# Optimization experiments

Measured on AMD Instinct MI355X. Metric: run time of the kernel, lower is better.

## Reference

```python
import jax, jax.numpy as jnp
import numpy as np

SEQ_LEN, INPUT_DIM, HIDDEN_DIM, NUM_CLASSES, BATCH = 512, 256, 1024, 128, 256


def setup_inputs() -> dict:
    key = jax.random.key(0)
    ks = jax.random.split(key, 12)
    sx = np.sqrt(2.0 / INPUT_DIM).astype(np.float32)
    sh = np.sqrt(2.0 / HIDDEN_DIM).astype(np.float32)
    inp = {
        "x": jax.random.randint(ks[0], (BATCH, SEQ_LEN, 1), 0, NUM_CLASSES, dtype=jnp.int32),
        "emb": jax.random.normal(ks[1], (NUM_CLASSES, INPUT_DIM), jnp.float32),
        "Wcx": jax.random.normal(ks[2], (HIDDEN_DIM, INPUT_DIM), jnp.float32) * sx,
        "bc": jnp.zeros((HIDDEN_DIM,), jnp.float32),
        "Wix": jax.random.normal(ks[3], (HIDDEN_DIM, INPUT_DIM), jnp.float32) * sx,
        "Wih": jax.random.normal(ks[4], (HIDDEN_DIM, HIDDEN_DIM), jnp.float32) * sh,
        "bi": jnp.zeros((HIDDEN_DIM,), jnp.float32),
        "Wfx": jax.random.normal(ks[5], (HIDDEN_DIM, INPUT_DIM), jnp.float32) * sx,
        "Wfh": jax.random.normal(ks[6], (HIDDEN_DIM, HIDDEN_DIM), jnp.float32) * sh,
        "bf": jnp.zeros((HIDDEN_DIM,), jnp.float32),
        "Wox": jax.random.normal(ks[7], (HIDDEN_DIM, INPUT_DIM), jnp.float32) * sx,
        "Woh": jax.random.normal(ks[8], (HIDDEN_DIM, HIDDEN_DIM), jnp.float32) * sh,
        "bo": jnp.zeros((HIDDEN_DIM,), jnp.float32),
        "Wph": jax.random.normal(ks[9], (NUM_CLASSES, HIDDEN_DIM), jnp.float32) * sh,
        "bp": jnp.zeros((NUM_CLASSES,), jnp.float32),
    }
    return inp


def reference(x, emb, Wcx, bc, Wix, Wih, bi, Wfx, Wfh, bf, Wox, Woh, bo, Wph, bp):
    B = x.shape[0]
    H = Wfh.shape[0]
    xt = emb[x[:, :, 0]]                       # [B, S, I] embedded inputs
    # Precompute the input-to-gate projections (parallel over time; identical math)
    xf = jnp.einsum("bsi,hi->sbh", xt, Wfx)    # [S, B, H]
    xi = jnp.einsum("bsi,hi->sbh", xt, Wix)
    xo = jnp.einsum("bsi,hi->sbh", xt, Wox)
    xc = jnp.einsum("bsi,hi->sbh", xt, Wcx)

    def step(carry, inputs):
        c, h = carry
        xf_t, xi_t, xo_t, xc_t = inputs
        # peephole gates read cell state c, not h
        f = jax.nn.sigmoid(xf_t + c @ Wfh.T + bf)
        i = jax.nn.sigmoid(xi_t + c @ Wih.T + bi)
        o = jax.nn.sigmoid(xo_t + c @ Woh.T + bo)
        c_new = jax.nn.sigmoid(xc_t + bc) * i + c * f
        h_new = jnp.tanh(c_new) * o
        return (c_new, h_new), None

    c0 = jnp.zeros((B, H), xt.dtype)
    h0 = jnp.zeros((B, H), xt.dtype)
    (c_T, h_T), _ = jax.lax.scan(step, (c0, h0), (xf, xi, xo, xc))
    p = h_T @ Wph.T + bp                       # [B, num_classes]
    return jax.nn.log_softmax(p, axis=1)
```

## Files before the change

kernel.cpp:

```cpp
#include <hip/hip_runtime.h>

#define SEQ  512
#define IDIM 256
#define H    1024
#define NC   128
#define B    256
#define NBLK 256

typedef __attribute__((ext_vector_type(8))) short bh8;
typedef __attribute__((ext_vector_type(4))) float f4;
typedef __attribute__((ext_vector_type(4))) int i4;

__device__ __forceinline__ float sigf(float x) { return 1.0f / (1.0f + __expf(-x)); }

__device__ __forceinline__ unsigned short bf16r(float v) {
    unsigned u = __builtin_bit_cast(unsigned, v);
    u += 0x7fffu + ((u >> 16) & 1u);
    return (unsigned short)(u >> 16);
}

__global__ __launch_bounds__(256) void tables_kernel(
    const float* __restrict__ emb,
    const float* __restrict__ Wcx, const float* __restrict__ bc,
    const float* __restrict__ Wix, const float* __restrict__ bi,
    const float* __restrict__ Wfx, const float* __restrict__ bf,
    const float* __restrict__ Wox, const float* __restrict__ bo,
    float* __restrict__ FF, float* __restrict__ II,
    float* __restrict__ OO, float* __restrict__ G)
{
    const int k = blockIdx.x;
    const int h = blockIdx.y * 256 + threadIdx.x;
    __shared__ float e[IDIM];
    e[threadIdx.x] = emb[k * IDIM + threadIdx.x];
    __syncthreads();
    const float4* e4  = (const float4*)e;
    const float4* wf4 = (const float4*)(Wfx + (size_t)h * IDIM);
    const float4* wi4 = (const float4*)(Wix + (size_t)h * IDIM);
    const float4* wo4 = (const float4*)(Wox + (size_t)h * IDIM);
    const float4* wc4 = (const float4*)(Wcx + (size_t)h * IDIM);
    float aF = 0.f, aI = 0.f, aO = 0.f, aC = 0.f;
#pragma unroll 4
    for (int i = 0; i < IDIM / 4; i++) {
        float4 ev = e4[i];
        float4 a = wf4[i]; aF += ev.x * a.x + ev.y * a.y + ev.z * a.z + ev.w * a.w;
        float4 b = wi4[i]; aI += ev.x * b.x + ev.y * b.y + ev.z * b.z + ev.w * b.w;
        float4 c = wo4[i]; aO += ev.x * c.x + ev.y * c.y + ev.z * c.z + ev.w * c.w;
        float4 d = wc4[i]; aC += ev.x * d.x + ev.y * d.y + ev.z * d.z + ev.w * d.w;
    }
    const int o = k * H + h;
    FF[o] = aF + bf[h];
    II[o] = aI + bi[h];
    OO[o] = aO + bo[h];
    G[o]  = sigf(aC + bc[h]);
}

__global__ __launch_bounds__(256) void swz_kernel(const float* __restrict__ W,
                                                  unsigned short* __restrict__ D)
{
    int g = blockIdx.x * 256 + threadIdx.x;
    int h  = g >> 7;
    int kc = (g & 127) << 3;
    const float4* s = (const float4*)(W + (size_t)h * H + kc);
    float4 a = s[0], b = s[1];
    unsigned short tmp[8] = { bf16r(a.x), bf16r(a.y), bf16r(a.z), bf16r(a.w),
                              bf16r(b.x), bf16r(b.y), bf16r(b.z), bf16r(b.w) };
    int nb = h >> 4, kb = kc >> 5, quad = (kc >> 3) & 3;
    int lane = (h & 15) + (quad << 4);
    bh8 v;
#pragma unroll
    for (int j = 0; j < 8; j++) v[j] = (short)tmp[j];
    *(bh8*)(D + (size_t)((nb * 32 + kb) * 512 + lane * 8)) = v;
}

__global__ __launch_bounds__(256, 1) void persist_kernel(
    const unsigned short* __restrict__ Wf, const unsigned short* __restrict__ Wi,
    const unsigned short* __restrict__ Wo,
    const float* __restrict__ FF, const float* __restrict__ II,
    const float* __restrict__ OO, const float* __restrict__ G,
    const int* __restrict__ x,
    unsigned short* c16a, unsigned short* c16b,
    float* __restrict__ hb, int* flags)
{
    const int blk = blockIdx.x;
    const int rt = blk >> 5;
    const int nt = blk & 31;
    const int tid  = threadIdx.x;
    const int wave = tid >> 6;
    const int lane = tid & 63;
    const int msub = wave & 1, nsub = wave >> 1;
    const int l15 = lane & 15, quad = lane >> 4;

    __shared__ unsigned short cs[32 * 1024];

    const int row0 = rt * 32;
    const int arow = msub * 16 + l15;
    const int abase = arow * 1024;
    const int asw = arow & 7;
    const int hcol = nt * 32 + nsub * 16 + l15;
    const int nb = nt * 2 + nsub;

    const unsigned short* wfp = Wf + (size_t)nb * 32 * 512 + (size_t)lane * 8;
    const unsigned short* wip = Wi + (size_t)nb * 32 * 512 + (size_t)lane * 8;
    const unsigned short* wop = Wo + (size_t)nb * 32 * 512 + (size_t)lane * 8;

    bh8 wf_r[32], wi_r[32];
#pragma unroll
    for (int kt = 0; kt < 32; kt++) {
        wf_r[kt] = *(const bh8*)(wfp + (size_t)kt * 512);
        wi_r[kt] = *(const bh8*)(wip + (size_t)kt * 512);
    }

    float cn_keep[4] = {0.f, 0.f, 0.f, 0.f};

    for (int s = 0; s < SEQ; s++) {
        const unsigned short* cur16 = (s & 1) ? c16b : c16a;
        unsigned short*       nxt16 = (s & 1) ? c16a : c16b;

        float ffv[4], iiv[4], ggv[4];
#pragma unroll
        for (int r = 0; r < 4; r++) {
            int b = row0 + msub * 16 + quad * 4 + r;
            int tok = x[b * SEQ + s];
            ffv[r] = FF[tok * H + hcol];
            iiv[r] = II[tok * H + hcol];
            ggv[r] = G[tok * H + hcol];
        }

        f4 accF = {0.f, 0.f, 0.f, 0.f}, accI = {0.f, 0.f, 0.f, 0.f};
        if (s > 0) {
            i4 tmp[16];
#pragma unroll
            for (int i = 0; i < 16; i++) {
                int chunk = i * 256 + tid;
                int row = chunk >> 7, g = chunk & 127;
                const i4* p = (const i4*)(cur16 + (size_t)(row0 + row) * H + g * 8);
                asm volatile("global_load_dwordx4 %0, %1, off sc0 sc1"
                             : "=v"(tmp[i]) : "v"(p));
            }
            asm volatile("s_waitcnt vmcnt(0)" ::: "memory");
#pragma unroll
            for (int i = 0; i < 16; i++) {
                int chunk = i * 256 + tid;
                int row = chunk >> 7, g = chunk & 127;
                *(i4*)(cs + row * 1024 + ((g ^ (row & 7)) << 3)) = tmp[i];
            }
            __syncthreads();
#pragma unroll
            for (int kt = 0; kt < 32; kt++) {
                bh8 a = *(const bh8*)(cs + abase + (((kt * 4 + quad) ^ asw) << 3));
                accF = __builtin_amdgcn_mfma_f32_16x16x32_bf16(a, wf_r[kt], accF, 0, 0, 0);
                accI = __builtin_amdgcn_mfma_f32_16x16x32_bf16(a, wi_r[kt], accI, 0, 0, 0);
            }
        }

#pragma unroll
        for (int r = 0; r < 4; r++) {
            float f = sigf(ffv[r] + accF[r]);
            float i = sigf(iiv[r] + accI[r]);
            float cn = ggv[r] * i + cn_keep[r] * f;
            cn_keep[r] = cn;
            int b = row0 + msub * 16 + quad * 4 + r;
            unsigned us = bf16r(cn);
            unsigned ot = (unsigned)__shfl_xor((int)us, 1);
            if (s < SEQ - 1 && (lane & 1) == 0)
                __hip_atomic_store((unsigned*)(nxt16 + (size_t)b * H + hcol), us | (ot << 16),
                                   __ATOMIC_RELAXED, __HIP_MEMORY_SCOPE_AGENT);
        }

        if (s < SEQ - 1) {
            __syncthreads();
            if (wave == 0) {
                if (lane == 0) {
                    int v = s + 1;
                    asm volatile("global_store_dword %0, %1, off sc0 sc1"
                                 :: "v"(&flags[blk]), "v"(v) : "memory");
                }
                const int target = s + 1;
                const int* pf = &flags[rt * 32 + (lane & 31)];
                int guard = 0;
                for (;;) {
                    int fv;
                    asm volatile("global_load_dword %0, %1, off sc0 sc1\n\ts_waitcnt vmcnt(0)"
                                 : "=v"(fv) : "v"(pf) : "memory");
                    if (__all(fv >= target)) break;
                    if (++guard > (1 << 20)) break;
                }
            }
            __syncthreads();
        }
    }

    f4 accO = {0.f, 0.f, 0.f, 0.f};
#pragma unroll 4
    for (int kt = 0; kt < 32; kt++) {
        bh8 a   = *(const bh8*)(cs + abase + (((kt * 4 + quad) ^ asw) << 3));
        bh8 bor = *(const bh8*)(wop + (size_t)kt * 512);
        accO = __builtin_amdgcn_mfma_f32_16x16x32_bf16(a, bor, accO, 0, 0, 0);
    }
#pragma unroll
    for (int r = 0; r < 4; r++) {
        int b = row0 + msub * 16 + quad * 4 + r;
        int tok = x[b * SEQ + (SEQ - 1)];
        float o = sigf(OO[tok * H + hcol] + accO[r]);
        hb[(size_t)b * H + hcol] = tanhf(cn_keep[r]) * o;
    }
}

__global__ __launch_bounds__(128) void out_kernel(
    const float* __restrict__ hbuf, const float* __restrict__ Wph,
    const float* __restrict__ bp, float* __restrict__ out)
{
    const int b = blockIdx.x;
    const int j = threadIdx.x;
    __shared__ float hs[H];
    for (int t = j; t < H; t += 128) hs[t] = hbuf[(size_t)b * H + t];
    __syncthreads();
    const float4* w4 = (const float4*)(Wph + (size_t)j * H);
    const float4* h4 = (const float4*)hs;
    float acc = bp[j];
#pragma unroll 4
    for (int k = 0; k < H / 4; k++) {
        float4 a = w4[k], v = h4[k];
        acc += a.x * v.x + a.y * v.y + a.z * v.z + a.w * v.w;
    }
    __shared__ float red[128];
    red[j] = acc; __syncthreads();
    for (int off = 64; off > 0; off >>= 1) { if (j < off) red[j] = fmaxf(red[j], red[j + off]); __syncthreads(); }
    float m = red[0]; __syncthreads();
    red[j] = __expf(acc - m); __syncthreads();
    for (int off = 64; off > 0; off >>= 1) { if (j < off) red[j] += red[j + off]; __syncthreads(); }
    float lse = m + __logf(red[0]);
    out[(size_t)b * NC + j] = acc - lse;
}

extern "C" void kernel_launch(void* const* d_in, const int* in_sizes, int n_in,
                              void* d_out, int out_size, void* d_ws, size_t ws_size,
                              hipStream_t stream)
{
    const int*   x   = (const int*)d_in[0];
    const float* emb = (const float*)d_in[1];
    const float* Wcx = (const float*)d_in[2];
    const float* bc  = (const float*)d_in[3];
    const float* Wix = (const float*)d_in[4];
    const float* Wih = (const float*)d_in[5];
    const float* bi  = (const float*)d_in[6];
    const float* Wfx = (const float*)d_in[7];
    const float* Wfh = (const float*)d_in[8];
    const float* bf  = (const float*)d_in[9];
    const float* Wox = (const float*)d_in[10];
    const float* Woh = (const float*)d_in[11];
    const float* bo  = (const float*)d_in[12];
    const float* Wph = (const float*)d_in[13];
    const float* bp  = (const float*)d_in[14];
    float* out = (float*)d_out;

    char* wsb = (char*)d_ws;
    float* FF = (float*)(wsb + 0);
    float* II = (float*)(wsb + (512 << 10));
    float* OO = (float*)(wsb + (1024 << 10));
    float* G  = (float*)(wsb + (1536 << 10));
    float* hb = (float*)(wsb + (2048 << 10));
    int*   flags = (int*)(wsb + (3072 << 10));
    unsigned short* Wf_sw = (unsigned short*)(wsb + (4096 << 10));
    unsigned short* Wi_sw = (unsigned short*)(wsb + (6144 << 10));
    unsigned short* Wo_sw = (unsigned short*)(wsb + (8192 << 10));
    unsigned short* c16a  = (unsigned short*)(wsb + (10240 << 10));
    unsigned short* c16b  = (unsigned short*)(wsb + (10752 << 10));

    hipMemsetAsync(flags, 0, NBLK * sizeof(int), stream);

    tables_kernel<<<dim3(NC, 4), 256, 0, stream>>>(emb, Wcx, bc, Wix, bi, Wfx, bf, Wox, bo,
                                                   FF, II, OO, G);
    swz_kernel<<<512, 256, 0, stream>>>(Wfh, Wf_sw);
    swz_kernel<<<512, 256, 0, stream>>>(Wih, Wi_sw);
    swz_kernel<<<512, 256, 0, stream>>>(Woh, Wo_sw);

    persist_kernel<<<NBLK, 256, 0, stream>>>(Wf_sw, Wi_sw, Wo_sw, FF, II, OO, G, x,
                                             c16a, c16b, hb, flags);

    out_kernel<<<B, 128, 0, stream>>>(hb, Wph, bp, out);
}
```

Before: 2.757 ms.

## Halve persistent blocks, use per-wave flags and drop block-level barrier handshake

The persistent LSTM kernel now runs 128 blocks, each covering 32 batch rows by 64 hidden columns, so every wave computes two 16-row M tiles and reuses its register-resident weights across both. The inter-block handshake moves from one flag per block, with two __syncthreads around a wave-0 spin, to one flag per wave. Each wave now spins on the 64 flags of its row group before loading, then publishes its own flag after a vmcnt wait. The goal is lower per-step synchronization latency and fewer blocks in the dependency chain, at the cost of twice the MFMA work per wave, more polling traffic, and half as many CUs in use.

```diff
diff --git a/kernel.cpp b/kernel.cpp
--- a/kernel.cpp
+++ b/kernel.cpp
@@ -5,7 +5,7 @@
 #define H    1024
 #define NC   128
 #define B    256
-#define NBLK 256
+#define NBLK 128
 
 typedef __attribute__((ext_vector_type(8))) short bh8;
 typedef __attribute__((ext_vector_type(4))) float f4;
@@ -82,22 +82,21 @@
     float* __restrict__ hb, int* flags)
 {
     const int blk = blockIdx.x;
-    const int rt = blk >> 5;
-    const int nt = blk & 31;
+    const int rt = blk >> 4;
+    const int nt = blk & 15;
     const int tid  = threadIdx.x;
     const int wave = tid >> 6;
     const int lane = tid & 63;
-    const int msub = wave & 1, nsub = wave >> 1;
     const int l15 = lane & 15, quad = lane >> 4;
 
     __shared__ unsigned short cs[32 * 1024];
 
     const int row0 = rt * 32;
-    const int arow = msub * 16 + l15;
-    const int abase = arow * 1024;
-    const int asw = arow & 7;
-    const int hcol = nt * 32 + nsub * 16 + l15;
-    const int nb = nt * 2 + nsub;
+    const int ab0 = l15 * 1024;
+    const int ab1 = (16 + l15) * 1024;
+    const int asw = l15 & 7;
+    const int hcol = nt * 64 + wave * 16 + l15;
+    const int nb = nt * 4 + wave;
 
     const unsigned short* wfp = Wf + (size_t)nb * 32 * 512 + (size_t)lane * 8;
     const unsigned short* wip = Wi + (size_t)nb * 32 * 512 + (size_t)lane * 8;
@@ -110,100 +109,113 @@
         wi_r[kt] = *(const bh8*)(wip + (size_t)kt * 512);
     }
 
-    float cn_keep[4] = {0.f, 0.f, 0.f, 0.f};
+    float cn_keep[2][4] = {{0.f,0.f,0.f,0.f},{0.f,0.f,0.f,0.f}};
+    int* const pf = flags + rt * 64 + lane;
+    int* const myflag = flags + rt * 64 + nt * 4 + wave;
 
     for (int s = 0; s < SEQ; s++) {
         const unsigned short* cur16 = (s & 1) ? c16b : c16a;
         unsigned short*       nxt16 = (s & 1) ? c16a : c16b;
 
-        float ffv[4], iiv[4], ggv[4];
-#pragma unroll
-        for (int r = 0; r < 4; r++) {
-            int b = row0 + msub * 16 + quad * 4 + r;
-            int tok = x[b * SEQ + s];
-            ffv[r] = FF[tok * H + hcol];
-            iiv[r] = II[tok * H + hcol];
-            ggv[r] = G[tok * H + hcol];
-        }
-
-        f4 accF = {0.f, 0.f, 0.f, 0.f}, accI = {0.f, 0.f, 0.f, 0.f};
+        float ffv[2][4], iiv[2][4], ggv[2][4];
+#pragma unroll
+        for (int mh = 0; mh < 2; mh++)
+#pragma unroll
+            for (int r = 0; r < 4; r++) {
+                int b = row0 + mh * 16 + quad * 4 + r;
+                int tok = x[b * SEQ + s];
+                ffv[mh][r] = FF[tok * H + hcol];
+                iiv[mh][r] = II[tok * H + hcol];
+                ggv[mh][r] = G[tok * H + hcol];
+            }
+
+        f4 accF[2] = {{0.f,0.f,0.f,0.f},{0.f,0.f,0.f,0.f}};
+        f4 accI[2] = {{0.f,0.f,0.f,0.f},{0.f,0.f,0.f,0.f}};
         if (s > 0) {
-            i4 tmp[16];
-#pragma unroll
-            for (int i = 0; i < 16; i++) {
-                int chunk = i * 256 + tid;
-                int row = chunk >> 7, g = chunk & 127;
-                const i4* p = (const i4*)(cur16 + (size_t)(row0 + row) * H + g * 8);
-                asm volatile("global_load_dwordx4 %0, %1, off sc0 sc1"
-                             : "=v"(tmp[i]) : "v"(p));
-            }
-            asm volatile("s_waitcnt vmcnt(0)" ::: "memory");
-#pragma unroll
-            for (int i = 0; i < 16; i++) {
-                int chunk = i * 256 + tid;
-                int row = chunk >> 7, g = chunk & 127;
-                *(i4*)(cs + row * 1024 + ((g ^ (row & 7)) << 3)) = tmp[i];
-            }
-            __syncthreads();
-#pragma unroll
-            for (int kt = 0; kt < 32; kt++) {
-                bh8 a = *(const bh8*)(cs + abase + (((kt * 4 + quad) ^ asw) << 3));
-                accF = __builtin_amdgcn_mfma_f32_16x16x32_bf16(a, wf_r[kt], accF, 0, 0, 0);
-                accI = __builtin_amdgcn_mfma_f32_16x16x32_bf16(a, wi_r[kt], accI, 0, 0, 0);
-            }
-        }
-
-#pragma unroll
-        for (int r = 0; r < 4; r++) {
-            float f = sigf(ffv[r] + accF[r]);
-            float i = sigf(iiv[r] + accI[r]);
-            float cn = ggv[r] * i + cn_keep[r] * f;
-            cn_keep[r] = cn;
-            int b = row0 + msub * 16 + quad * 4 + r;
-            unsigned us = bf16r(cn);
-            unsigned ot = (unsigned)__shfl_xor((int)us, 1);
-            if (s < SEQ - 1 && (lane & 1) == 0)
-                __hip_atomic_store((unsigned*)(nxt16 + (size_t)b * H + hcol), us | (ot << 16),
-                                   __ATOMIC_RELAXED, __HIP_MEMORY_SCOPE_AGENT);
-        }
-
-        if (s < SEQ - 1) {
-            __syncthreads();
-            if (wave == 0) {
-                if (lane == 0) {
-                    int v = s + 1;
-                    asm volatile("global_store_dword %0, %1, off sc0 sc1"
-                                 :: "v"(&flags[blk]), "v"(v) : "memory");
-                }
-                const int target = s + 1;
-                const int* pf = &flags[rt * 32 + (lane & 31)];
+            {
                 int guard = 0;
                 for (;;) {
                     int fv;
                     asm volatile("global_load_dword %0, %1, off sc0 sc1\n\ts_waitcnt vmcnt(0)"
                                  : "=v"(fv) : "v"(pf) : "memory");
-                    if (__all(fv >= target)) break;
+                    if (__all(fv >= s)) break;
                     if (++guard > (1 << 20)) break;
                 }
             }
+            i4 tmp[16];
+#pragma unroll
+            for (int i = 0; i < 16; i++) {
+                int idx = i * 64 + lane;
+                int row = wave * 8 + (idx >> 7), g = idx & 127;
+                const i4* p = (const i4*)(cur16 + (size_t)(row0 + row) * H + g * 8);
+                asm volatile("global_load_dwordx4 %0, %1, off sc0 sc1"
+                             : "=v"(tmp[i]) : "v"(p));
+            }
+            asm volatile("s_waitcnt vmcnt(0)" ::: "memory");
+#pragma unroll
+            for (int i = 0; i < 16; i++) {
+                int idx = i * 64 + lane;
+                int row = wave * 8 + (idx >> 7), g = idx & 127;
+                *(i4*)(cs + row * 1024 + ((g ^ (row & 7)) << 3)) = tmp[i];
+            }
             __syncthreads();
+#pragma unroll
+            for (int kt = 0; kt < 32; kt++) {
+                int off = ((kt * 4 + quad) ^ asw) << 3;
+                bh8 a0 = *(const bh8*)(cs + ab0 + off);
+                bh8 a1 = *(const bh8*)(cs + ab1 + off);
+                accF[0] = __builtin_amdgcn_mfma_f32_16x16x32_bf16(a0, wf_r[kt], accF[0], 0, 0, 0);
+                accF[1] = __builtin_amdgcn_mfma_f32_16x16x32_bf16(a1, wf_r[kt], accF[1], 0, 0, 0);
+                accI[0] = __builtin_amdgcn_mfma_f32_16x16x32_bf16(a0, wi_r[kt], accI[0], 0, 0, 0);
+                accI[1] = __builtin_amdgcn_mfma_f32_16x16x32_bf16(a1, wi_r[kt], accI[1], 0, 0, 0);
+            }
         }
-    }
-
-    f4 accO = {0.f, 0.f, 0.f, 0.f};
+
+#pragma unroll
+        for (int mh = 0; mh < 2; mh++)
+#pragma unroll
+            for (int r = 0; r < 4; r++) {
+                float f = sigf(ffv[mh][r] + accF[mh][r]);
+                float i = sigf(iiv[mh][r] + accI[mh][r]);
+                float cn = ggv[mh][r] * i + cn_keep[mh][r] * f;
+                cn_keep[mh][r] = cn;
+                int b = row0 + mh * 16 + quad * 4 + r;
+                unsigned us = bf16r(cn);
+                unsigned ot = (unsigned)__shfl_xor((int)us, 1);
+                if (s < SEQ - 1 && (lane & 1) == 0)
+                    __hip_atomic_store((unsigned*)(nxt16 + (size_t)b * H + hcol), us | (ot << 16),
+                                       __ATOMIC_RELAXED, __HIP_MEMORY_SCOPE_AGENT);
+            }
+
+        if (s < SEQ - 1) {
+            asm volatile("s_waitcnt vmcnt(0)" ::: "memory");
+            if (lane == 0) {
+                int v = s + 1;
+                asm volatile("global_store_dword %0, %1, off sc0 sc1"
+                             :: "v"(myflag), "v"(v) : "memory");
+            }
+        }
+    }
+
+    f4 accO[2] = {{0.f,0.f,0.f,0.f},{0.f,0.f,0.f,0.f}};
 #pragma unroll 4
     for (int kt = 0; kt < 32; kt++) {
-        bh8 a   = *(const bh8*)(cs + abase + (((kt * 4 + quad) ^ asw) << 3));
-        bh8 bor = *(const bh8*)(wop + (size_t)kt * 512);
-        accO = __builtin_amdgcn_mfma_f32_16x16x32_bf16(a, bor, accO, 0, 0, 0);
-    }
-#pragma unroll
-    for (int r = 0; r < 4; r++) {
-        int b = row0 + msub * 16 + quad * 4 + r;
-        int tok = x[b * SEQ + (SEQ - 1)];
-        float o = sigf(OO[tok * H + hcol] + accO[r]);
-        hb[(size_t)b * H + hcol] = tanhf(cn_keep[r]) * o;
-    }
+        int off = ((kt * 4 + quad) ^ asw) << 3;
+        bh8 a0 = *(const bh8*)(cs + ab0 + off);
+        bh8 a1 = *(const bh8*)(cs + ab1 + off);
+        bh8 bo = *(const bh8*)(wop + (size_t)kt * 512);
+        accO[0] = __builtin_amdgcn_mfma_f32_16x16x32_bf16(a0, bo, accO[0], 0, 0, 0);
+        accO[1] = __builtin_amdgcn_mfma_f32_16x16x32_bf16(a1, bo, accO[1], 0, 0, 0);
+    }
+#pragma unroll
+    for (int mh = 0; mh < 2; mh++)
+#pragma unroll
+        for (int r = 0; r < 4; r++) {
+            int b = row0 + mh * 16 + quad * 4 + r;
+            int tok = x[b * SEQ + (SEQ - 1)];
+            float o = sigf(OO[tok * H + hcol] + accO[mh][r]);
+            hb[(size_t)b * H + hcol] = tanhf(cn_keep[mh][r]) * o;
+        }
 }
 
 __global__ __launch_bounds__(128) void out_kernel(
@@ -267,7 +279,7 @@
     unsigned short* c16a  = (unsigned short*)(wsb + (10240 << 10));
     unsigned short* c16b  = (unsigned short*)(wsb + (10752 << 10));
 
-    hipMemsetAsync(flags, 0, NBLK * sizeof(int), stream);
+    hipMemsetAsync(flags, 0, 2048, stream);
 
     tables_kernel<<<dim3(NC, 4), 256, 0, stream>>>(emb, Wcx, bc, Wix, bi, Wfx, bf, Wox, bo,
                                                    FF, II, OO, G);
```

Result: slower. 3.428 ms (+24.3%).
